# Kernel tuning notes

Measured on AMD Instinct MI355X. Metric: run time of the kernel, lower is better.

## Reference

```python
import jax, jax.numpy as jnp
import numpy as np
import math

B, N, D = 4, 4096, 256


def setup_inputs() -> dict:
    key = jax.random.key(0)
    k0, k1, k2, k3 = jax.random.split(key, 4)
    # kaiming-uniform-like init for the square weight matrices
    bound = math.sqrt(6.0 / D)
    return {
        "x": jax.random.normal(k0, (B, N, D), dtype=jnp.float32),
        "Wq": jax.random.uniform(k1, (D, D), dtype=jnp.float32, minval=-bound, maxval=bound),
        "Wk": jax.random.uniform(k2, (D, D), dtype=jnp.float32, minval=-bound, maxval=bound),
        "Wv": jax.random.uniform(k3, (D, D), dtype=jnp.float32, minval=-bound, maxval=bound),
    }


def reference(x, Wq, Wk, Wv):
    # x: [B, N, D]; W*: [D, D]
    q = x @ Wq.T
    k = x @ Wk.T
    v = x @ Wv.T
    n = x.shape[1]
    d_k = x.shape[2]
    # mask = triu(ones, diagonal=1): 1 strictly above the diagonal.
    # (1 - mask) is 1 on and below the diagonal, so those positions get -1e10
    # (faithful to the original: it masks the diagonal and past, keeps future).
    mask = jnp.triu(jnp.ones((n, n), dtype=x.dtype), k=1)
    scale = jnp.asarray(1.0 / math.sqrt(d_k), dtype=x.dtype)
    s = (jnp.einsum('bnd,bmd->bnm', q, k) - (1.0 - mask) * 1e10) * scale
    # Faithful quirk: softmax over dim=1 (the query/row axis), not the last axis.
    s = jax.nn.softmax(s, axis=1)
    return jnp.einsum('bnm,bmd->bnd', s, v)
```

## Files before the change

### kernel.cpp

```cpp
#include <hip/hip_runtime.h>
#include <hip/hip_bf16.h>


typedef float f32x4 __attribute__((ext_vector_type(4)));
typedef __bf16 bf16x8 __attribute__((ext_vector_type(8)));
typedef __bf16 bf16x4 __attribute__((ext_vector_type(4)));

#define MFMA16(a, b, c) __builtin_amdgcn_mfma_f32_16x16x32_bf16((a), (b), (c), 0, 0, 0)

constexpr int SEQ = 4096;
constexpr int DIM = 256;

__host__ __device__ inline int tri(int x) { return (x * (x + 1)) >> 1; }

__device__ __forceinline__ void gl16(const __bf16* g, __bf16* l) {
  __builtin_amdgcn_global_load_lds((const __attribute__((address_space(1))) void*)g,
                                   (__attribute__((address_space(3))) void*)l, 16, 0, 0);
}

__global__ void k_prep(const float* __restrict__ Wq, const float* __restrict__ Wk,
                       const float* __restrict__ Wv, __bf16* __restrict__ Wb,
                       float* __restrict__ colsum) {
  int i = blockIdx.x * 256 + threadIdx.x;
  if (i < 3 * 65536) {
    const float* src = (i < 65536) ? Wq : (i < 131072 ? Wk : Wv);
    Wb[i] = (__bf16)src[i & 65535];
  }
  if (i < 4 * SEQ) colsum[i] = 0.f;
}

__global__ __launch_bounds__(256, 2) void k_qkv(const float* __restrict__ x,
                                                const __bf16* __restrict__ Wb,
                                                __bf16* __restrict__ Qb,
                                                __bf16* __restrict__ Kb,
                                                __bf16* __restrict__ Vb) {
  __shared__ __bf16 wsh[64][264];
  const int t = threadIdx.x, lane = t & 63, w = t >> 6;
  const int ln = lane & 15, quad = lane >> 4, q8 = quad * 8;
  const int i0 = blockIdx.x * 64;
  bf16x8 xa[8];
#pragma unroll
  for (int kf = 0; kf < 8; ++kf) {
    const float* src = &x[(size_t)(i0 + w * 16 + ln) * DIM + kf * 32 + q8];
    float4 v0 = *(const float4*)&src[0];
    float4 v1 = *(const float4*)&src[4];
    xa[kf] = bf16x8{(__bf16)v0.x, (__bf16)v0.y, (__bf16)v0.z, (__bf16)v0.w,
                    (__bf16)v1.x, (__bf16)v1.y, (__bf16)v1.z, (__bf16)v1.w};
  }
  for (int zj = 0; zj < 12; ++zj) {
    const int z = zj >> 2, j0 = (zj & 3) * 64;
    const __bf16* W = Wb + z * 65536 + j0 * 256;
    bf16x8 stg[8];
#pragma unroll
    for (int i = 0; i < 8; ++i) stg[i] = *(const bf16x8*)&W[(t + i * 256) * 8];
    __syncthreads();
#pragma unroll
    for (int i = 0; i < 8; ++i)
      *(bf16x8*)&wsh[(t >> 5) + i * 8][(t & 31) * 8] = stg[i];
    __syncthreads();
    f32x4 acc[4] = {};
#pragma unroll
    for (int kf = 0; kf < 8; ++kf) {
      bf16x8 bb[4];
#pragma unroll
      for (int tj = 0; tj < 4; ++tj)
        bb[tj] = *(bf16x8*)&wsh[tj * 16 + ln][kf * 32 + q8];
#pragma unroll
      for (int tj = 0; tj < 4; ++tj) acc[tj] = MFMA16(xa[kf], bb[tj], acc[tj]);
    }
    __bf16* Out = (z == 0) ? Qb : (z == 1 ? Kb : Vb);
#pragma unroll
    for (int tj = 0; tj < 4; ++tj)
#pragma unroll
      for (int r = 0; r < 4; ++r) {
        int row = i0 + w * 16 + quad * 4 + r;
        int col = j0 + tj * 16 + ln;
        Out[(size_t)row * DIM + col] = (__bf16)acc[tj][r];
      }
  }
}

__global__ __launch_bounds__(256, 2) void k_scores(const __bf16* __restrict__ Qb,
                                                   const __bf16* __restrict__ Kb,
                                                   __bf16* __restrict__ E,
                                                   float* __restrict__ colsum,
                                                   int mtLo, int triLo, int ntiles) {
  __shared__ __bf16 qsh[2 * 64 * 256];
  const int t = threadIdx.x, lane = t & 63, w = t >> 6;
  const int ln = lane & 15, quad = lane >> 4, q8 = quad * 8;
  const int bid = blockIdx.x;
  const int b = (bid & 7) >> 1;
  const int rest = ((bid >> 3) << 1) | (bid & 1);
  const int mt = mtLo + (rest >> 2);
  const int s = rest & 3;
  if (s > mt) return;
  const int m0 = mt * 64;
  const __bf16* Qp = Qb + (size_t)b * SEQ * DIM;
  const __bf16* Kp = Kb + (size_t)b * SEQ * DIM;
  bf16x8 kb[8];
#pragma unroll
  for (int kf = 0; kf < 8; ++kf)
    kb[kf] = *(const bf16x8*)&Kp[(size_t)(m0 + w * 16 + ln) * DIM + kf * 32 + q8];
  auto stageq = [&](int ncv, int buf) {
    const __bf16* src = Qp + (size_t)ncv * 16384;
#pragma unroll
    for (int i2 = 0; i2 < 8; ++i2) {
      int sl = t + i2 * 256;
      int row = sl >> 5, g = sl & 31;
      gl16(&src[row * 256 + ((g ^ (row & 15)) << 3)], &qsh[buf * 16384 + sl * 8]);
    }
  };
  float csum4[4] = {0.f, 0.f, 0.f, 0.f};
  const int P16 = w * 2 + (quad >> 1);
  const int sub = (quad & 1) * 4;
  int nc = s, cur = 0;
  if (nc <= mt) stageq(nc, 0);
  for (; nc <= mt; nc += 4, cur ^= 1) {
    __syncthreads();
    if (nc + 4 <= mt) stageq(nc + 4, cur ^ 1);
    f32x4 accST[4] = {};
#pragma unroll
    for (int kf = 0; kf < 8; ++kf) {
#pragma unroll
      for (int tn = 0; tn < 4; ++tn) {
        int row = tn * 16 + ln;
        bf16x8 bq = *(const bf16x8*)&qsh[cur * 16384 + row * 256 +
                                         (((kf * 4 + quad) ^ ln) << 3)];
        accST[tn] = MFMA16(kb[kf], bq, accST[tn]);
      }
    }
    __bf16* Et = E + ((size_t)b * ntiles + (tri(mt) - triLo) + nc) * 4096;
#pragma unroll
    for (int tn = 0; tn < 4; ++tn) {
      int nl = tn * 16 + ln;
      int n_g = nc * 64 + nl;
      int mb = m0 + w * 16 + quad * 4;
      bf16x4 pk;
#pragma unroll
      for (int r = 0; r < 4; ++r) {
        float e = (n_g < mb + r) ? __expf(accST[tn][r] * 0.0625f) : 0.f;
        csum4[r] += e;
        pk[r] = (__bf16)e;
      }
      *(bf16x4*)&Et[nl * 64 + ((P16 ^ (nl & 7)) << 3) + sub] = pk;
    }
  }
#pragma unroll
  for (int r = 0; r < 4; ++r) {
    float v = csum4[r];
    v += __shfl_xor(v, 1);
    v += __shfl_xor(v, 2);
    v += __shfl_xor(v, 4);
    v += __shfl_xor(v, 8);
    if (ln == 0) atomicAdd(&colsum[b * SEQ + m0 + w * 16 + quad * 4 + r], v);
  }
}

__global__ void k_vpt(const __bf16* __restrict__ Vb, const float* __restrict__ colsum,
                      __bf16* __restrict__ VpT, int mtLo) {
  __shared__ __bf16 tile[64][72];
  const int t = threadIdx.x;
  const int b = blockIdx.z;
  const int mblk = mtLo + blockIdx.x;
  const int m0 = mblk * 64, d0 = blockIdx.y * 64;
  {
    int row = t >> 2, part = t & 3;
    float cs = colsum[b * SEQ + m0 + row];
    float inv = (m0 + row == 0) ? (1.0f / 4096.0f) : (1.0f / cs);
#pragma unroll
    for (int i = 0; i < 2; ++i) {
      int c = part * 2 + i;
      bf16x8 v = *(const bf16x8*)&Vb[(size_t)(b * SEQ + m0 + row) * DIM + d0 + c * 8];
      bf16x8 o;
#pragma unroll
      for (int j = 0; j < 8; ++j) o[j] = (__bf16)((float)v[j] * inv);
      *(bf16x8*)&tile[row][c * 8] = o;
    }
  }
  __syncthreads();
  {
    int row = t >> 2, part = t & 3;
#pragma unroll
    for (int i = 0; i < 2; ++i) {
      int c = part * 2 + i;
      bf16x8 o;
#pragma unroll
      for (int j = 0; j < 8; ++j) o[j] = tile[c * 8 + j][row];
      *(bf16x8*)&VpT[(size_t)((b * 64 + mblk) * 256 + d0 + row) * 64 +
                     ((c ^ (row & 7)) << 3)] = o;
    }
  }
}

__global__ __launch_bounds__(256, 4) void k_pv(const __bf16* __restrict__ E,
                                               const __bf16* __restrict__ VpT,
                                               const __bf16* __restrict__ Vb,
                                               float* __restrict__ out,
                                               int mtLo, int mtHi, int triLo,
                                               int ntiles) {
  __shared__ __bf16 esh[2 * 32 * 64];
  __shared__ __bf16 vsh[2 * 128 * 64];
  const int t = threadIdx.x, lane = t & 63, w = t >> 6;
  const int ln = lane & 15, quad = lane >> 4;
  const int bid = blockIdx.x;
  const int b = (bid & 7) >> 1;
  const int idx = ((bid >> 3) << 1) | (bid & 1);
  const int p = idx >> 1, dh = idx & 1;
  const int nt32 = (p & 1) ? (2 * mtHi - 1 - (p >> 1)) : (p >> 1);
  const int nc = nt32 >> 1, half = nt32 & 1;
  const int mtStart = (nc > mtLo) ? nc : mtLo;
  const int n0 = nt32 * 32;
  const __bf16* Vt = VpT + (size_t)b * SEQ * DIM;
  auto stageE = [&](int msv, int buf) {
    const __bf16* ep =
        E + ((size_t)b * ntiles + (tri(msv) - triLo) + nc) * 4096 + half * 2048;
    gl16(&ep[t * 8], &esh[buf * 2048 + t * 8]);
  };
  auto stageVp = [&](int msv, int buf) {
    const __bf16* vp = Vt + (size_t)msv * 16384 + dh * 8192;
#pragma unroll
    for (int i2 = 0; i2 < 4; ++i2) {
      int sl = t + i2 * 256;
      gl16(&vp[sl * 8], &vsh[buf * 8192 + sl * 8]);
    }
  };
  f32x4 accO[2][2] = {};
  int cur = 0;
  stageE(mtHi - 1, 0);
  stageVp(mtHi - 1, 0);
  for (int ms = mtHi - 1; ms >= mtStart; --ms, cur ^= 1) {
    __syncthreads();
    if (ms - 1 >= mtStart) { stageE(ms - 1, cur ^ 1); stageVp(ms - 1, cur ^ 1); }
#pragma unroll
    for (int kf = 0; kf < 2; ++kf) {
      bf16x8 aa[2], bb[2];
#pragma unroll
      for (int tn = 0; tn < 2; ++tn) {
        int row = tn * 16 + ln;
        aa[tn] = *(const bf16x8*)&esh[cur * 2048 + row * 64 +
                                      (((kf * 4 + quad) ^ (row & 7)) << 3)];
      }
#pragma unroll
      for (int td = 0; td < 2; ++td) {
        int rl = w * 32 + td * 16 + ln;
        bb[td] = *(const bf16x8*)&vsh[cur * 8192 + rl * 64 +
                                      (((kf * 4 + quad) ^ (rl & 7)) << 3)];
      }
#pragma unroll
      for (int tn = 0; tn < 2; ++tn)
#pragma unroll
        for (int td = 0; td < 2; ++td)
          accO[tn][td] = MFMA16(aa[tn], bb[td], accO[tn][td]);
    }
  }
  float* Op = out + ((size_t)b << 20);
  const __bf16* V0 = Vb + ((size_t)b << 20);
  const bool init = (nc >= mtLo);
#pragma unroll
  for (int tn = 0; tn < 2; ++tn)
#pragma unroll
    for (int td = 0; td < 2; ++td) {
      int col = dh * 128 + w * 32 + td * 16 + ln;
      float c0 = init ? (float)V0[col] * (1.0f / 4096.0f) : 0.f;
#pragma unroll
      for (int r = 0; r < 4; ++r) {
        int row = n0 + tn * 16 + quad * 4 + r;
        float* pp = &Op[(size_t)row * DIM + col];
        float v = accO[tn][td][r] + c0;
        if (!init) v += *pp;
        *pp = v;
      }
    }
}

extern "C" void kernel_launch(void* const* d_in, const int* in_sizes, int n_in,
                              void* d_out, int out_size, void* d_ws, size_t ws_size,
                              hipStream_t stream) {
  const float* x = (const float*)d_in[0];
  const float* Wq = (const float*)d_in[1];
  const float* Wk = (const float*)d_in[2];
  const float* Wv = (const float*)d_in[3];
  float* out = (float*)d_out;
  char* ws = (char*)d_ws;
  __bf16* Qb = (__bf16*)(ws);
  __bf16* Kb = (__bf16*)(ws + (8u << 20));
  __bf16* Vb = (__bf16*)(ws + (16u << 20));
  __bf16* VpT = (__bf16*)(ws + (24u << 20));
  float* colsum = (float*)(ws + (32u << 20));
  __bf16* Wb = (__bf16*)(ws + (32u << 20) + (1u << 16));
  const size_t base2 = (32u << 20) + (1u << 16) + (384u << 10);
  __bf16* E = (__bf16*)(ws + base2);
  const size_t fullE = (size_t)4 * 2080 * 4096 * sizeof(__bf16);
  int nPass, lo[3], hi[3];
  if (ws_size >= base2 + fullE) {
    nPass = 1; lo[0] = 0; hi[0] = 64;
  } else {
    nPass = 3;
    lo[0] = 0;  hi[0] = 37;
    lo[1] = 37; hi[1] = 53;
    lo[2] = 53; hi[2] = 64;
  }

  k_prep<<<dim3(768), dim3(256), 0, stream>>>(Wq, Wk, Wv, Wb, colsum);
  k_qkv<<<dim3(256), dim3(256), 0, stream>>>(x, Wb, Qb, Kb, Vb);
  for (int p = 0; p < nPass; ++p) {
    const int nmt = hi[p] - lo[p];
    const int triLo = tri(lo[p]);
    const int ntiles = tri(hi[p]) - triLo;
    k_scores<<<dim3(16 * nmt), dim3(256), 0, stream>>>(Qb, Kb, E, colsum,
                                                       lo[p], triLo, ntiles);
    k_vpt<<<dim3(nmt, 4, 4), dim3(256), 0, stream>>>(Vb, colsum, VpT, lo[p]);
    k_pv<<<dim3(16 * hi[p]), dim3(256), 0, stream>>>(E, VpT, Vb, out,
                                                     lo[p], hi[p], triLo, ntiles);
  }
}
```

Baseline: 179.6 us.

## Load V fragments directly to registers and deepen E staging pipeline in k_pv

The PV kernel stops staging the V tile through LDS. Each wave now loads its B-operand fragments straight from global memory into registers, using two register sets that alternate between steps. E tiles move to a 4-deep LDS ring buffer, with a manual vmcnt wait, raw s_barrier and setprio around the MFMAs, so loads for later steps overlap with compute. This removes the V LDS traffic and round-trip, and lets more blocks fit by shrinking LDS use. The cost is uncoalesced-ish global fragment loads, higher register pressure, and a hand-tuned waitcnt whose correctness depends on the exact load count per step.

```diff
diff --git a/kernel.cpp b/kernel.cpp
--- a/kernel.cpp
+++ b/kernel.cpp
@@ -198,8 +198,7 @@
                                                float* __restrict__ out,
                                                int mtLo, int mtHi, int triLo,
                                                int ntiles) {
-  __shared__ __bf16 esh[2 * 32 * 64];
-  __shared__ __bf16 vsh[2 * 128 * 64];
+  __shared__ __bf16 esh[4 * 32 * 64];
   const int t = threadIdx.x, lane = t & 63, w = t >> 6;
   const int ln = lane & 15, quad = lane >> 4;
   const int bid = blockIdx.x;
@@ -216,43 +215,64 @@
         E + ((size_t)b * ntiles + (tri(msv) - triLo) + nc) * 4096 + half * 2048;
     gl16(&ep[t * 8], &esh[buf * 2048 + t * 8]);
   };
-  auto stageVp = [&](int msv, int buf) {
+  auto loadbb = [&](bf16x8 (&BB)[2][2], int msv) {
     const __bf16* vp = Vt + (size_t)msv * 16384 + dh * 8192;
 #pragma unroll
-    for (int i2 = 0; i2 < 4; ++i2) {
-      int sl = t + i2 * 256;
-      gl16(&vp[sl * 8], &vsh[buf * 8192 + sl * 8]);
-    }
+    for (int kf = 0; kf < 2; ++kf)
+#pragma unroll
+      for (int td = 0; td < 2; ++td) {
+        int rl = w * 32 + td * 16 + ln;
+        BB[kf][td] = *(const bf16x8*)&vp[rl * 64 +
+                                         (((kf * 4 + quad) ^ (rl & 7)) << 3)];
+      }
   };
   f32x4 accO[2][2] = {};
-  int cur = 0;
-  stageE(mtHi - 1, 0);
-  stageVp(mtHi - 1, 0);
-  for (int ms = mtHi - 1; ms >= mtStart; --ms, cur ^= 1) {
-    __syncthreads();
-    if (ms - 1 >= mtStart) { stageE(ms - 1, cur ^ 1); stageVp(ms - 1, cur ^ 1); }
-#pragma unroll
-    for (int kf = 0; kf < 2; ++kf) {
-      bf16x8 aa[2], bb[2];
-#pragma unroll
-      for (int tn = 0; tn < 2; ++tn) {
-        int row = tn * 16 + ln;
-        aa[tn] = *(const bf16x8*)&esh[cur * 2048 + row * 64 +
-                                      (((kf * 4 + quad) ^ (row & 7)) << 3)];
-      }
-#pragma unroll
-      for (int td = 0; td < 2; ++td) {
-        int rl = w * 32 + td * 16 + ln;
-        bb[td] = *(const bf16x8*)&vsh[cur * 8192 + rl * 64 +
-                                      (((kf * 4 + quad) ^ (rl & 7)) << 3)];
-      }
-#pragma unroll
-      for (int tn = 0; tn < 2; ++tn)
-#pragma unroll
-        for (int td = 0; td < 2; ++td)
-          accO[tn][td] = MFMA16(aa[tn], bb[td], accO[tn][td]);
-    }
-  }
+  bf16x8 bbA[2][2], bbB[2][2];
+  const int ms0 = mtHi - 1;
+  const int T = mtHi - mtStart;
+  auto clampm = [&](int m) { return m < mtStart ? mtStart : m; };
+  stageE(ms0, 0);
+  loadbb(bbA, ms0);
+  stageE(clampm(ms0 - 1), 1);
+  loadbb(bbB, clampm(ms0 - 1));
+  stageE(clampm(ms0 - 2), 2);
+  int ms = ms0, bcur = 0;
+
+#define PV_STEP(BBSET)                                                        \
+  {                                                                           \
+    asm volatile("s_waitcnt vmcnt(6)" ::: "memory");                          \
+    __builtin_amdgcn_sched_barrier(0);                                        \
+    __builtin_amdgcn_s_barrier();                                             \
+    __builtin_amdgcn_sched_barrier(0);                                        \
+    const __bf16* eb = &esh[bcur * 2048];                                     \
+    bf16x8 aa[2][2];                                                          \
+    _Pragma("unroll") for (int kf = 0; kf < 2; ++kf)                          \
+      _Pragma("unroll") for (int tn = 0; tn < 2; ++tn) {                      \
+        int row = tn * 16 + ln;                                               \
+        aa[kf][tn] = *(const bf16x8*)&eb[row * 64 +                           \
+                                         (((kf * 4 + quad) ^ (row & 7)) << 3)]; \
+      }                                                                       \
+    __builtin_amdgcn_s_setprio(1);                                            \
+    _Pragma("unroll") for (int kf = 0; kf < 2; ++kf)                          \
+      _Pragma("unroll") for (int tn = 0; tn < 2; ++tn)                        \
+        _Pragma("unroll") for (int td = 0; td < 2; ++td)                      \
+          accO[tn][td] = MFMA16(aa[kf][tn], BBSET[kf][td], accO[tn][td]);     \
+    __builtin_amdgcn_s_setprio(0);                                            \
+    loadbb(BBSET, clampm(ms - 2));           \
+    stageE(clampm(ms - 3), (bcur + 3) & 3);               \
+    bcur = (bcur + 1) & 3;                                                    \
+    --ms;                                                                     \
+  }
+
+  int i = 0;
+  for (; i + 2 <= T; i += 2) {
+    PV_STEP(bbA);
+    PV_STEP(bbB);
+  }
+  if (i < T) PV_STEP(bbA);
+#undef PV_STEP
+  asm volatile("s_waitcnt vmcnt(0)" ::: "memory");
+
   float* Op = out + ((size_t)b << 20);
   const __bf16* V0 = Vb + ((size_t)b << 20);
   const bool init = (nc >= mtLo);
```

Result: slower. 187.1 us (+4.2%).

## Recompute scores in fused PV kernel instead of materializing exp matrix

Applied to the files above, without the earlier changes.

The scores kernel now only accumulates column sums and no longer writes the bf16 exp matrix E to global memory. A new fused kernel recomputes Q·K^T per 64-row tile using 32x32 MFMA, exponentiates into LDS, and multiplies by the pre-normalized V in the same loop, writing output directly. This removes the large E round-trip and the multi-pass workspace splitting, at the cost of computing QK^T twice. The fused kernel runs only 256 blocks with single-buffered K staging and a serial loop of up to 64 tiles per block, so load imbalance and low occupancy are risks.

```diff
diff --git a/kernel.cpp b/kernel.cpp
--- a/kernel.cpp
+++ b/kernel.cpp
@@ -3,15 +3,15 @@
 
 
 typedef float f32x4 __attribute__((ext_vector_type(4)));
+typedef float f32x16 __attribute__((ext_vector_type(16)));
 typedef __bf16 bf16x8 __attribute__((ext_vector_type(8)));
 typedef __bf16 bf16x4 __attribute__((ext_vector_type(4)));
 
 #define MFMA16(a, b, c) __builtin_amdgcn_mfma_f32_16x16x32_bf16((a), (b), (c), 0, 0, 0)
+#define MFMA32(a, b, c) __builtin_amdgcn_mfma_f32_32x32x16_bf16((a), (b), (c), 0, 0, 0)
 
 constexpr int SEQ = 4096;
 constexpr int DIM = 256;
-
-__host__ __device__ inline int tri(int x) { return (x * (x + 1)) >> 1; }
 
 __device__ __forceinline__ void gl16(const __bf16* g, __bf16* l) {
   __builtin_amdgcn_global_load_lds((const __attribute__((address_space(1))) void*)g,
@@ -80,18 +80,16 @@
   }
 }
 
-__global__ __launch_bounds__(256, 2) void k_scores(const __bf16* __restrict__ Qb,
-                                                   const __bf16* __restrict__ Kb,
-                                                   __bf16* __restrict__ E,
-                                                   float* __restrict__ colsum,
-                                                   int mtLo, int triLo, int ntiles) {
+__global__ __launch_bounds__(256, 2) void k_scoresA(const __bf16* __restrict__ Qb,
+                                                    const __bf16* __restrict__ Kb,
+                                                    float* __restrict__ colsum) {
   __shared__ __bf16 qsh[2 * 64 * 256];
   const int t = threadIdx.x, lane = t & 63, w = t >> 6;
   const int ln = lane & 15, quad = lane >> 4, q8 = quad * 8;
   const int bid = blockIdx.x;
   const int b = (bid & 7) >> 1;
   const int rest = ((bid >> 3) << 1) | (bid & 1);
-  const int mt = mtLo + (rest >> 2);
+  const int mt = rest >> 2;
   const int s = rest & 3;
   if (s > mt) return;
   const int m0 = mt * 64;
@@ -111,8 +109,6 @@
     }
   };
   float csum4[4] = {0.f, 0.f, 0.f, 0.f};
-  const int P16 = w * 2 + (quad >> 1);
-  const int sub = (quad & 1) * 4;
   int nc = s, cur = 0;
   if (nc <= mt) stageq(nc, 0);
   for (; nc <= mt; nc += 4, cur ^= 1) {
@@ -129,20 +125,15 @@
         accST[tn] = MFMA16(kb[kf], bq, accST[tn]);
       }
     }
-    __bf16* Et = E + ((size_t)b * ntiles + (tri(mt) - triLo) + nc) * 4096;
 #pragma unroll
     for (int tn = 0; tn < 4; ++tn) {
-      int nl = tn * 16 + ln;
-      int n_g = nc * 64 + nl;
+      int n_g = nc * 64 + tn * 16 + ln;
       int mb = m0 + w * 16 + quad * 4;
-      bf16x4 pk;
 #pragma unroll
       for (int r = 0; r < 4; ++r) {
         float e = (n_g < mb + r) ? __expf(accST[tn][r] * 0.0625f) : 0.f;
         csum4[r] += e;
-        pk[r] = (__bf16)e;
-      }
-      *(bf16x4*)&Et[nl * 64 + ((P16 ^ (nl & 7)) << 3) + sub] = pk;
+      }
     }
   }
 #pragma unroll
@@ -192,83 +183,103 @@
   }
 }
 
-__global__ __launch_bounds__(256, 4) void k_pv(const __bf16* __restrict__ E,
-                                               const __bf16* __restrict__ VpT,
-                                               const __bf16* __restrict__ Vb,
-                                               float* __restrict__ out,
-                                               int mtLo, int mtHi, int triLo,
-                                               int ntiles) {
-  __shared__ __bf16 esh[2 * 32 * 64];
-  __shared__ __bf16 vsh[2 * 128 * 64];
+__global__ __launch_bounds__(256, 2) void k_fused(const __bf16* __restrict__ Qb,
+                                                  const __bf16* __restrict__ Kb,
+                                                  const __bf16* __restrict__ VpT,
+                                                  const __bf16* __restrict__ Vb,
+                                                  float* __restrict__ out) {
+  __shared__ __bf16 ksh[64 * 256];
+  __shared__ __bf16 psh[64 * 64];
   const int t = threadIdx.x, lane = t & 63, w = t >> 6;
   const int ln = lane & 15, quad = lane >> 4;
+  const int l32 = lane & 31, hi = lane >> 5;
   const int bid = blockIdx.x;
   const int b = (bid & 7) >> 1;
-  const int idx = ((bid >> 3) << 1) | (bid & 1);
-  const int p = idx >> 1, dh = idx & 1;
-  const int nt32 = (p & 1) ? (2 * mtHi - 1 - (p >> 1)) : (p >> 1);
-  const int nc = nt32 >> 1, half = nt32 & 1;
-  const int mtStart = (nc > mtLo) ? nc : mtLo;
-  const int n0 = nt32 * 32;
+  const int pp = ((bid >> 3) << 1) | (bid & 1);
+  const int NT = (pp & 1) ? (63 - (pp >> 1)) : (pp >> 1);
+  const int n0 = NT * 64;
+  const __bf16* Qp = Qb + (size_t)b * SEQ * DIM;
+  const __bf16* Kp = Kb + (size_t)b * SEQ * DIM;
   const __bf16* Vt = VpT + (size_t)b * SEQ * DIM;
-  auto stageE = [&](int msv, int buf) {
-    const __bf16* ep =
-        E + ((size_t)b * ntiles + (tri(msv) - triLo) + nc) * 4096 + half * 2048;
-    gl16(&ep[t * 8], &esh[buf * 2048 + t * 8]);
+  const int tm = w >> 1, tn32 = w & 1;
+  bf16x8 qb[16];
+#pragma unroll
+  for (int kf = 0; kf < 16; ++kf)
+    qb[kf] = *(const bf16x8*)&Qp[(size_t)(n0 + tn32 * 32 + l32) * DIM + kf * 16 + hi * 8];
+  auto stagek = [&](int ms) {
+    const __bf16* src = Kp + (size_t)ms * 16384;
+#pragma unroll
+    for (int i2 = 0; i2 < 8; ++i2) {
+      int sl = t + i2 * 256;
+      int row = sl >> 5, g = sl & 31;
+      gl16(&src[row * 256 + ((g ^ (row & 15)) << 3)], &ksh[sl * 8]);
+    }
   };
-  auto stageVp = [&](int msv, int buf) {
-    const __bf16* vp = Vt + (size_t)msv * 16384 + dh * 8192;
-#pragma unroll
-    for (int i2 = 0; i2 < 4; ++i2) {
-      int sl = t + i2 * 256;
-      gl16(&vp[sl * 8], &vsh[buf * 8192 + sl * 8]);
-    }
-  };
-  f32x4 accO[2][2] = {};
-  int cur = 0;
-  stageE(mtHi - 1, 0);
-  stageVp(mtHi - 1, 0);
-  for (int ms = mtHi - 1; ms >= mtStart; --ms, cur ^= 1) {
-    __syncthreads();
-    if (ms - 1 >= mtStart) { stageE(ms - 1, cur ^ 1); stageVp(ms - 1, cur ^ 1); }
-#pragma unroll
-    for (int kf = 0; kf < 2; ++kf) {
-      bf16x8 aa[2], bb[2];
-#pragma unroll
-      for (int tn = 0; tn < 2; ++tn) {
-        int row = tn * 16 + ln;
-        aa[tn] = *(const bf16x8*)&esh[cur * 2048 + row * 64 +
-                                      (((kf * 4 + quad) ^ (row & 7)) << 3)];
-      }
-#pragma unroll
-      for (int td = 0; td < 2; ++td) {
-        int rl = w * 32 + td * 16 + ln;
-        bb[td] = *(const bf16x8*)&vsh[cur * 8192 + rl * 64 +
-                                      (((kf * 4 + quad) ^ (rl & 7)) << 3)];
-      }
-#pragma unroll
-      for (int tn = 0; tn < 2; ++tn)
-#pragma unroll
-        for (int td = 0; td < 2; ++td)
-          accO[tn][td] = MFMA16(aa[tn], bb[td], accO[tn][td]);
+  f32x4 accO[4][4] = {};
+  stagek(NT);
+  for (int ms = NT; ms < 64; ++ms) {
+    __syncthreads();
+    f32x16 accS = {};
+#pragma unroll
+    for (int kf = 0; kf < 16; ++kf) {
+      int mrow = tm * 32 + l32;
+      bf16x8 ka = *(const bf16x8*)&ksh[mrow * 256 +
+                                       (((kf * 2 + hi) ^ (mrow & 15)) << 3)];
+      accS = MFMA32(ka, qb[kf], accS);
+    }
+    {
+      int nrow = tn32 * 32 + l32;
+      int n_gl = n0 + nrow;
+#pragma unroll
+      for (int rr = 0; rr < 4; ++rr) {
+        int mbase = ms * 64 + tm * 32 + rr * 8 + hi * 4;
+        bf16x4 pk;
+#pragma unroll
+        for (int r = 0; r < 4; ++r) {
+          float e = (n_gl < mbase + r) ? __expf(accS[rr * 4 + r] * 0.0625f) : 0.f;
+          pk[r] = (__bf16)e;
+        }
+        int p8 = tm * 4 + rr;
+        *(bf16x4*)&psh[nrow * 64 + ((p8 ^ (nrow & 7)) << 3) + hi * 4] = pk;
+      }
+    }
+    __syncthreads();
+    if (ms + 1 < 64) stagek(ms + 1);
+    const __bf16* vp = Vt + (size_t)ms * 16384;
+    bf16x8 bb[2][4];
+#pragma unroll
+    for (int kf = 0; kf < 2; ++kf)
+#pragma unroll
+      for (int td = 0; td < 4; ++td) {
+        int d = w * 64 + td * 16 + ln;
+        bb[kf][td] = *(const bf16x8*)&vp[d * 64 + (((kf * 4 + quad) ^ (d & 7)) << 3)];
+      }
+#pragma unroll
+    for (int t16 = 0; t16 < 4; ++t16) {
+      int row = t16 * 16 + ln;
+      bf16x8 pa[2];
+#pragma unroll
+      for (int kf = 0; kf < 2; ++kf)
+        pa[kf] = *(const bf16x8*)&psh[row * 64 + (((kf * 4 + quad) ^ (row & 7)) << 3)];
+#pragma unroll
+      for (int td = 0; td < 4; ++td)
+#pragma unroll
+        for (int kf = 0; kf < 2; ++kf)
+          accO[t16][td] = MFMA16(pa[kf], bb[kf][td], accO[t16][td]);
     }
   }
   float* Op = out + ((size_t)b << 20);
   const __bf16* V0 = Vb + ((size_t)b << 20);
-  const bool init = (nc >= mtLo);
-#pragma unroll
-  for (int tn = 0; tn < 2; ++tn)
-#pragma unroll
-    for (int td = 0; td < 2; ++td) {
-      int col = dh * 128 + w * 32 + td * 16 + ln;
-      float c0 = init ? (float)V0[col] * (1.0f / 4096.0f) : 0.f;
+#pragma unroll
+  for (int t16 = 0; t16 < 4; ++t16)
+#pragma unroll
+    for (int td = 0; td < 4; ++td) {
+      int col = w * 64 + td * 16 + ln;
+      float c0 = (float)V0[col] * (1.0f / 4096.0f);
 #pragma unroll
       for (int r = 0; r < 4; ++r) {
-        int row = n0 + tn * 16 + quad * 4 + r;
-        float* pp = &Op[(size_t)row * DIM + col];
-        float v = accO[tn][td][r] + c0;
-        if (!init) v += *pp;
-        *pp = v;
+        int row = n0 + t16 * 16 + quad * 4 + r;
+        Op[(size_t)row * DIM + col] = accO[t16][td][r] + c0;
       }
     }
 }
@@ -288,29 +299,10 @@
   __bf16* VpT = (__bf16*)(ws + (24u << 20));
   float* colsum = (float*)(ws + (32u << 20));
   __bf16* Wb = (__bf16*)(ws + (32u << 20) + (1u << 16));
-  const size_t base2 = (32u << 20) + (1u << 16) + (384u << 10);
-  __bf16* E = (__bf16*)(ws + base2);
-  const size_t fullE = (size_t)4 * 2080 * 4096 * sizeof(__bf16);
-  int nPass, lo[3], hi[3];
-  if (ws_size >= base2 + fullE) {
-    nPass = 1; lo[0] = 0; hi[0] = 64;
-  } else {
-    nPass = 3;
-    lo[0] = 0;  hi[0] = 37;
-    lo[1] = 37; hi[1] = 53;
-    lo[2] = 53; hi[2] = 64;
-  }
 
   k_prep<<<dim3(768), dim3(256), 0, stream>>>(Wq, Wk, Wv, Wb, colsum);
   k_qkv<<<dim3(256), dim3(256), 0, stream>>>(x, Wb, Qb, Kb, Vb);
-  for (int p = 0; p < nPass; ++p) {
-    const int nmt = hi[p] - lo[p];
-    const int triLo = tri(lo[p]);
-    const int ntiles = tri(hi[p]) - triLo;
-    k_scores<<<dim3(16 * nmt), dim3(256), 0, stream>>>(Qb, Kb, E, colsum,
-                                                       lo[p], triLo, ntiles);
-    k_vpt<<<dim3(nmt, 4, 4), dim3(256), 0, stream>>>(Vb, colsum, VpT, lo[p]);
-    k_pv<<<dim3(16 * hi[p]), dim3(256), 0, stream>>>(E, VpT, Vb, out,
-                                                     lo[p], hi[p], triLo, ntiles);
-  }
-}
+  k_scoresA<<<dim3(16 * 64), dim3(256), 0, stream>>>(Qb, Kb, colsum);
+  k_vpt<<<dim3(64, 4, 4), dim3(256), 0, stream>>>(Vb, colsum, VpT, 0);
+  k_fused<<<dim3(256), dim3(256), 0, stream>>>(Qb, Kb, VpT, Vb, out);
+}
```

Result: slower. 235.9 us (+31.3%).
